# Optimization experiments

Measured on AMD Instinct MI355X. Metric: run time of the kernel, lower is better.

The kernel has to match this reference:

```python
import jax, jax.numpy as jnp
import numpy as np

COMMITMENT_COST = 0.25


def setup_inputs() -> dict:
    key = jax.random.key(0)
    k1, k2 = jax.random.split(key)
    B, L, D, K = 32, 1024, 128, 1024
    z = jax.random.normal(k1, (B, L, D), dtype=jnp.float32)
    # torch init: uniform_(-1/num_embeddings, 1/num_embeddings)
    codebook = jax.random.uniform(k2, (K, D), dtype=jnp.float32,
                                  minval=-1.0 / K, maxval=1.0 / K)
    return {"z": z, "codebook": codebook}


def reference(z, codebook):
    D = codebook.shape[1]
    flat_z = z.reshape(-1, D)                         # [N, D]
    # squared-euclidean distances, expanded form (same math as torch)
    distances = (jnp.sum(flat_z ** 2, axis=1, keepdims=True)
                 + jnp.sum(codebook ** 2, axis=1)
                 - 2.0 * flat_z @ codebook.T)         # [N, K]
    encoding_indices = jnp.argmin(distances, axis=1)  # [N]
    quantized = codebook[encoding_indices].reshape(z.shape)
    # straight-through estimator
    z_q = z + jax.lax.stop_gradient(quantized - z)
    q_loss = jnp.mean((jax.lax.stop_gradient(quantized) - z) ** 2)
    e_loss = jnp.mean((quantized - jax.lax.stop_gradient(z)) ** 2)
    vq_loss = q_loss + COMMITMENT_COST * e_loss
    return z_q, vq_loss, encoding_indices
```

## Files before the change

kernel.cpp:

```cpp
#include <hip/hip_runtime.h>
#include <float.h>

#define NTOK 32768
#define DDIM 128
#define KCODES 1024
#define TT 128
#define KC 64
#define NCHUNK (KCODES / KC)
#define NTHR 512

typedef __attribute__((ext_vector_type(8))) short short8v;
typedef __attribute__((ext_vector_type(4))) float f32x4;

__device__ __forceinline__ float nofuse(float x) { asm volatile("" : "+v"(x)); return x; }

__device__ __forceinline__ unsigned short bf16rne(float x) {
    unsigned int u = __float_as_uint(x);
    unsigned int r = u + 0x7FFFu + ((u >> 16) & 1u);
    return (unsigned short)(r >> 16);
}
__device__ __forceinline__ float bf16tof(unsigned short h) {
    return __uint_as_float(((unsigned int)h) << 16);
}

__device__ __forceinline__ void cvt8(const float* f, uint4& hw, uint4& lw) {
    unsigned int h[8], l[8];
    #pragma unroll
    for (int e = 0; e < 8; ++e) {
        unsigned short hh = bf16rne(f[e]);
        unsigned short ll = bf16rne(f[e] - bf16tof(hh));
        h[e] = hh; l[e] = ll;
    }
    hw = make_uint4(h[0] | (h[1] << 16), h[2] | (h[3] << 16),
                    h[4] | (h[5] << 16), h[6] | (h[7] << 16));
    lw = make_uint4(l[0] | (l[1] << 16), l[2] | (l[3] << 16),
                    l[4] | (l[5] << 16), l[6] | (l[7] << 16));
}

__global__ void rownorm_np(const float* __restrict__ a, float* __restrict__ out, int nrows) {
    int row = blockIdx.x * blockDim.x + threadIdx.x;
    if (row >= nrows) return;
    const float* p = a + (size_t)row * DDIM;
    float r[8];
    #pragma unroll
    for (int j = 0; j < 8; ++j) { float v = p[j]; r[j] = nofuse(v * v); }
    #pragma unroll
    for (int i = 8; i < DDIM; i += 8) {
        #pragma unroll
        for (int j = 0; j < 8; ++j) {
            float v = p[i + j];
            r[j] = nofuse(r[j] + nofuse(v * v));
        }
    }
    float s01 = nofuse(r[0] + r[1]);
    float s23 = nofuse(r[2] + r[3]);
    float s45 = nofuse(r[4] + r[5]);
    float s67 = nofuse(r[6] + r[7]);
    out[row] = nofuse(nofuse(s01 + s23) + nofuse(s45 + s67));
}

__global__ __launch_bounds__(NTHR, 2)
void dist_argmin(const float* __restrict__ z, const float* __restrict__ cb,
                 const float* __restrict__ cnorm,
                 float* __restrict__ zq, float* __restrict__ idxf_out,
                 float* __restrict__ partials) {
    __shared__ __align__(16) char smem[2 * 32768 + 2 * 16384 + 512];
    char* ztH = smem;
    char* ztL = smem + 32768;
    char* ctH = smem + 65536;
    char* ctL = smem + 65536 + 16384;
    float* zn_s = (float*)(smem + 65536 + 32768);
    float* red_v = (float*)ctH;
    int*   red_i = (int*)(ctH + 2048);
    int*   bidx  = (int*)(ctH + 4096);

    const int tid  = threadIdx.x;
    const int lane = tid & 63;
    const int wave = tid >> 6;
    const int wy   = wave & 3;
    const int wx   = wave >> 2;
    const int l15  = lane & 15;
    const int l4   = lane >> 4;
    const int t0   = blockIdx.x * TT;

    float4 pf[4];
    #pragma unroll
    for (int it = 0; it < 2; ++it) {
        int gd = it * NTHR + tid;
        int row = gd >> 4, slot = gd & 15;
        const float* g = cb + (size_t)row * DDIM + slot * 8;
        pf[2 * it]     = *(const float4*)g;
        pf[2 * it + 1] = *(const float4*)(g + 4);
    }

    #pragma unroll
    for (int it = 0; it < 4; ++it) {
        int g = it * NTHR + tid;
        int row = g >> 4, d8 = g & 15;
        const float* p = z + (size_t)(t0 + row) * DDIM + d8 * 8;
        float4 a = *(const float4*)p;
        float4 b = *(const float4*)(p + 4);
        float f[8] = {a.x, a.y, a.z, a.w, b.x, b.y, b.z, b.w};
        uint4 hw, lw;
        cvt8(f, hw, lw);
        int off = row * 256 + ((d8 << 4) ^ ((row & 7) << 4));
        *(uint4*)(ztH + off) = hw;
        *(uint4*)(ztL + off) = lw;
    }

    if (tid < TT) {
        const float* p = z + (size_t)(t0 + tid) * DDIM;
        float r[8];
        {
            float4 a = *(const float4*)p, b = *(const float4*)(p + 4);
            float v[8] = {a.x, a.y, a.z, a.w, b.x, b.y, b.z, b.w};
            #pragma unroll
            for (int j = 0; j < 8; ++j) r[j] = nofuse(v[j] * v[j]);
        }
        #pragma unroll
        for (int i = 8; i < DDIM; i += 8) {
            float4 a = *(const float4*)(p + i), b = *(const float4*)(p + i + 4);
            float v[8] = {a.x, a.y, a.z, a.w, b.x, b.y, b.z, b.w};
            #pragma unroll
            for (int j = 0; j < 8; ++j) r[j] = nofuse(r[j] + nofuse(v[j] * v[j]));
        }
        float s01 = nofuse(r[0] + r[1]), s23 = nofuse(r[2] + r[3]);
        float s45 = nofuse(r[4] + r[5]), s67 = nofuse(r[6] + r[7]);
        zn_s[tid] = nofuse(nofuse(s01 + s23) + nofuse(s45 + s67));
    }
    __syncthreads();

    short8v Ah[2][4], Al[2][4];
    #pragma unroll
    for (int tf = 0; tf < 2; ++tf) {
        int row = wy * 32 + tf * 16 + l15;
        int swz = (row & 7) << 4;
        #pragma unroll
        for (int ks = 0; ks < 4; ++ks) {
            int off = row * 256 + ((ks * 64 + (l4 << 4)) ^ swz);
            Ah[tf][ks] = *(const short8v*)(ztH + off);
            Al[tf][ks] = *(const short8v*)(ztL + off);
        }
    }
    float znr[8];
    #pragma unroll
    for (int tf = 0; tf < 2; ++tf)
        #pragma unroll
        for (int rg = 0; rg < 4; ++rg)
            znr[tf * 4 + rg] = zn_s[wy * 32 + tf * 16 + l4 * 4 + rg];

    float minv[8]; int mini[8];
    #pragma unroll
    for (int i = 0; i < 8; ++i) { minv[i] = FLT_MAX; mini[i] = 0; }

    for (int cc = 0; cc < NCHUNK; ++cc) {
        const int kc = cc * KC;
        __syncthreads();
        #pragma unroll
        for (int it = 0; it < 2; ++it) {
            int gd = it * NTHR + tid;
            int row = gd >> 4, slot = gd & 15;
            float f[8] = {pf[2*it].x, pf[2*it].y, pf[2*it].z, pf[2*it].w,
                          pf[2*it+1].x, pf[2*it+1].y, pf[2*it+1].z, pf[2*it+1].w};
            uint4 hw, lw;
            cvt8(f, hw, lw);
            int off = row * 256 + ((slot << 4) ^ ((row & 7) << 4));
            *(uint4*)(ctH + off) = hw;
            *(uint4*)(ctL + off) = lw;
        }
        __syncthreads();
        if (cc + 1 < NCHUNK) {
            #pragma unroll
            for (int it = 0; it < 2; ++it) {
                int gd = it * NTHR + tid;
                int row = gd >> 4, slot = gd & 15;
                const float* g = cb + (size_t)(kc + KC + row) * DDIM + slot * 8;
                pf[2 * it]     = *(const float4*)g;
                pf[2 * it + 1] = *(const float4*)(g + 4);
            }
        }

        f32x4 acc[2][2];
        #pragma unroll
        for (int tf = 0; tf < 2; ++tf)
            #pragma unroll
            for (int cf = 0; cf < 2; ++cf)
                acc[tf][cf] = (f32x4){0.f, 0.f, 0.f, 0.f};

        #pragma unroll
        for (int ks = 0; ks < 4; ++ks) {
            short8v Bh[2], Bl[2];
            #pragma unroll
            for (int cf = 0; cf < 2; ++cf) {
                int row = wx * 32 + cf * 16 + l15;
                int off = row * 256 + ((ks * 64 + (l4 << 4)) ^ ((row & 7) << 4));
                Bh[cf] = *(const short8v*)(ctH + off);
                Bl[cf] = *(const short8v*)(ctL + off);
            }
            #pragma unroll
            for (int tf = 0; tf < 2; ++tf)
                #pragma unroll
                for (int cf = 0; cf < 2; ++cf) {
                    acc[tf][cf] = __builtin_amdgcn_mfma_f32_16x16x32_bf16(Ah[tf][ks], Bh[cf], acc[tf][cf], 0, 0, 0);
                    acc[tf][cf] = __builtin_amdgcn_mfma_f32_16x16x32_bf16(Ah[tf][ks], Bl[cf], acc[tf][cf], 0, 0, 0);
                    acc[tf][cf] = __builtin_amdgcn_mfma_f32_16x16x32_bf16(Al[tf][ks], Bh[cf], acc[tf][cf], 0, 0, 0);
                }
        }

        #pragma unroll
        for (int cf = 0; cf < 2; ++cf) {
            int kk = kc + wx * 32 + cf * 16 + l15;
            float cn = cnorm[kk];
            #pragma unroll
            for (int tf = 0; tf < 2; ++tf)
                #pragma unroll
                for (int rg = 0; rg < 4; ++rg) {
                    float s = nofuse(znr[tf * 4 + rg] + cn);
                    float dist = fmaf(-2.0f, acc[tf][cf][rg], s);
                    int ii = tf * 4 + rg;
                    if (dist < minv[ii]) { minv[ii] = dist; mini[ii] = kk; }
                }
        }
    }

    __syncthreads();
    #pragma unroll
    for (int i = 0; i < 8; ++i) {
        float bv = minv[i]; int bi = mini[i];
        #pragma unroll
        for (int off = 1; off < 16; off <<= 1) {
            float ov = __shfl_xor(bv, off);
            int   oi = __shfl_xor(bi, off);
            if (ov < bv || (ov == bv && oi < bi)) { bv = ov; bi = oi; }
        }
        if (l15 == 0) {
            int tok = wy * 32 + (i >> 2) * 16 + l4 * 4 + (i & 3);
            red_v[tok * 2 + wx] = bv;
            red_i[tok * 2 + wx] = bi;
        }
    }
    __syncthreads();
    if (tid < TT) {
        float bv = red_v[tid * 2]; int bi = red_i[tid * 2];
        float v1 = red_v[tid * 2 + 1]; int i1 = red_i[tid * 2 + 1];
        if (v1 < bv || (v1 == bv && i1 < bi)) { bv = v1; bi = i1; }
        bidx[tid] = bi;
        idxf_out[t0 + tid] = (float)bi;
    }
    __syncthreads();

    float s = 0.0f;
    #pragma unroll
    for (int ft = 0; ft < 8; ++ft) {
        int g = ft * NTHR + tid;
        int t = g >> 5;
        int d4 = g & 31;
        int k = bidx[t];
        float4 q4 = *(const float4*)(cb + (size_t)k * DDIM + 4 * d4);
        float4 z4 = *(const float4*)(z + (size_t)(t0 + t) * DDIM + 4 * d4);
        *(float4*)(zq + (size_t)(t0 + t) * DDIM + 4 * d4) = q4;
        float dx = q4.x - z4.x, dy = q4.y - z4.y, dz = q4.z - z4.z, dw = q4.w - z4.w;
        s += dx * dx + dy * dy + dz * dz + dw * dw;
    }
    #pragma unroll
    for (int off = 32; off > 0; off >>= 1) s += __shfl_down(s, off);
    __shared__ float sm[8];
    if ((tid & 63) == 0) sm[tid >> 6] = s;
    __syncthreads();
    if (tid == 0) {
        float tot = 0.0f;
        #pragma unroll
        for (int w = 0; w < 8; ++w) tot += sm[w];
        partials[blockIdx.x] = tot;
    }
}

__global__ void loss_final(const float* __restrict__ partials, float* __restrict__ out_loss) {
    double s = 0.0;
    for (int i = threadIdx.x; i < NTOK / TT; i += 256) s += (double)partials[i];
    #pragma unroll
    for (int off = 32; off > 0; off >>= 1) s += __shfl_down(s, off);
    __shared__ double sm[4];
    int lane = threadIdx.x & 63, wv = threadIdx.x >> 6;
    if (lane == 0) sm[wv] = s;
    __syncthreads();
    if (threadIdx.x == 0) {
        double tot = sm[0] + sm[1] + sm[2] + sm[3];
        out_loss[0] = (float)(tot * 1.25 / (double)((size_t)NTOK * DDIM));
    }
}

extern "C" void kernel_launch(void* const* d_in, const int* in_sizes, int n_in,
                              void* d_out, int out_size, void* d_ws, size_t ws_size,
                              hipStream_t stream) {
    const float* z  = (const float*)d_in[0];
    const float* cb = (const float*)d_in[1];
    float* out = (float*)d_out;
    float* zq   = out;
    float* loss = out + (size_t)NTOK * DDIM;
    float* idxf = loss + 1;

    float* cnorm    = (float*)d_ws;
    float* partials = cnorm + KCODES;

    rownorm_np<<<KCODES / 256, 256, 0, stream>>>(cb, cnorm, KCODES);
    dist_argmin<<<NTOK / TT, NTHR, 0, stream>>>(z, cb, cnorm, zq, idxf, partials);
    loss_final<<<1, 256, 0, stream>>>(partials, loss);
}
```

Before: 131.7 us.

## Pre-pack codebook to bf16 hi/lo in global, load MFMA operands directly to registers

Result: slower. 158.1 us (+20.0%).

```diff
diff --git a/kernel.cpp b/kernel.cpp
--- a/kernel.cpp
+++ b/kernel.cpp
@@ -5,8 +5,6 @@
 #define DDIM 128
 #define KCODES 1024
 #define TT 128
-#define KC 64
-#define NCHUNK (KCODES / KC)
 #define NTHR 512
 
 typedef __attribute__((ext_vector_type(8))) short short8v;
@@ -37,42 +35,60 @@
                     l[4] | (l[5] << 16), l[6] | (l[7] << 16));
 }
 
-__global__ void rownorm_np(const float* __restrict__ a, float* __restrict__ out, int nrows) {
-    int row = blockIdx.x * blockDim.x + threadIdx.x;
-    if (row >= nrows) return;
-    const float* p = a + (size_t)row * DDIM;
-    float r[8];
-    #pragma unroll
-    for (int j = 0; j < 8; ++j) { float v = p[j]; r[j] = nofuse(v * v); }
-    #pragma unroll
-    for (int i = 8; i < DDIM; i += 8) {
-        #pragma unroll
-        for (int j = 0; j < 8; ++j) {
-            float v = p[i + j];
-            r[j] = nofuse(r[j] + nofuse(v * v));
-        }
-    }
-    float s01 = nofuse(r[0] + r[1]);
-    float s23 = nofuse(r[2] + r[3]);
-    float s45 = nofuse(r[4] + r[5]);
-    float s67 = nofuse(r[6] + r[7]);
-    out[row] = nofuse(nofuse(s01 + s23) + nofuse(s45 + s67));
+__device__ __forceinline__ short8v as_s8(uint4 v) { return __builtin_bit_cast(short8v, v); }
+
+__global__ __launch_bounds__(256)
+void pack_cb(const float* __restrict__ cb, float* __restrict__ cnorm,
+             ushort* __restrict__ cbh, ushort* __restrict__ cbl) {
+    const int tid = threadIdx.x;
+    const int b = blockIdx.x;
+    {
+        int row = b * 256 + tid;
+        const float* p = cb + (size_t)row * DDIM;
+        float r[8];
+        {
+            float4 a = *(const float4*)p, c = *(const float4*)(p + 4);
+            float v[8] = {a.x, a.y, a.z, a.w, c.x, c.y, c.z, c.w};
+            #pragma unroll
+            for (int j = 0; j < 8; ++j) r[j] = nofuse(v[j] * v[j]);
+        }
+        #pragma unroll
+        for (int i = 8; i < DDIM; i += 8) {
+            float4 a = *(const float4*)(p + i), c = *(const float4*)(p + i + 4);
+            float v[8] = {a.x, a.y, a.z, a.w, c.x, c.y, c.z, c.w};
+            #pragma unroll
+            for (int j = 0; j < 8; ++j) r[j] = nofuse(r[j] + nofuse(v[j] * v[j]));
+        }
+        float s01 = nofuse(r[0] + r[1]), s23 = nofuse(r[2] + r[3]);
+        float s45 = nofuse(r[4] + r[5]), s67 = nofuse(r[6] + r[7]);
+        cnorm[row] = nofuse(nofuse(s01 + s23) + nofuse(s45 + s67));
+    }
+    #pragma unroll
+    for (int it = 0; it < 16; ++it) {
+        int g = it * 256 + tid;
+        int row = b * 256 + (g >> 4);
+        int d8 = g & 15;
+        const float* q = cb + (size_t)row * DDIM + d8 * 8;
+        float4 a = *(const float4*)q, c = *(const float4*)(q + 4);
+        float f[8] = {a.x, a.y, a.z, a.w, c.x, c.y, c.z, c.w};
+        uint4 hw, lw;
+        cvt8(f, hw, lw);
+        *(uint4*)(cbh + (size_t)row * DDIM + d8 * 8) = hw;
+        *(uint4*)(cbl + (size_t)row * DDIM + d8 * 8) = lw;
+    }
 }
 
 __global__ __launch_bounds__(NTHR, 2)
 void dist_argmin(const float* __restrict__ z, const float* __restrict__ cb,
                  const float* __restrict__ cnorm,
+                 const ushort* __restrict__ cbh, const ushort* __restrict__ cbl,
                  float* __restrict__ zq, float* __restrict__ idxf_out,
                  float* __restrict__ partials) {
-    __shared__ __align__(16) char smem[2 * 32768 + 2 * 16384 + 512];
-    char* ztH = smem;
-    char* ztL = smem + 32768;
-    char* ctH = smem + 65536;
-    char* ctL = smem + 65536 + 16384;
-    float* zn_s = (float*)(smem + 65536 + 32768);
-    float* red_v = (float*)ctH;
-    int*   red_i = (int*)(ctH + 2048);
-    int*   bidx  = (int*)(ctH + 4096);
+    __shared__ float zn_s[TT];
+    __shared__ float red_v[TT * 2];
+    __shared__ int   red_i[TT * 2];
+    __shared__ int   bidx[TT];
+    __shared__ float sm[8];
 
     const int tid  = threadIdx.x;
     const int lane = tid & 63;
@@ -83,44 +99,36 @@
     const int l4   = lane >> 4;
     const int t0   = blockIdx.x * TT;
 
-    float4 pf[4];
-    #pragma unroll
-    for (int it = 0; it < 2; ++it) {
-        int gd = it * NTHR + tid;
-        int row = gd >> 4, slot = gd & 15;
-        const float* g = cb + (size_t)row * DDIM + slot * 8;
-        pf[2 * it]     = *(const float4*)g;
-        pf[2 * it + 1] = *(const float4*)(g + 4);
-    }
-
-    #pragma unroll
-    for (int it = 0; it < 4; ++it) {
-        int g = it * NTHR + tid;
-        int row = g >> 4, d8 = g & 15;
-        const float* p = z + (size_t)(t0 + row) * DDIM + d8 * 8;
-        float4 a = *(const float4*)p;
-        float4 b = *(const float4*)(p + 4);
-        float f[8] = {a.x, a.y, a.z, a.w, b.x, b.y, b.z, b.w};
-        uint4 hw, lw;
-        cvt8(f, hw, lw);
-        int off = row * 256 + ((d8 << 4) ^ ((row & 7) << 4));
-        *(uint4*)(ztH + off) = hw;
-        *(uint4*)(ztL + off) = lw;
+    short8v Ah[2][4], Al[2][4];
+    #pragma unroll
+    for (int tf = 0; tf < 2; ++tf) {
+        int row = t0 + wy * 32 + tf * 16 + l15;
+        const float* p = z + (size_t)row * DDIM;
+        #pragma unroll
+        for (int ks = 0; ks < 4; ++ks) {
+            float4 a = *(const float4*)(p + ks * 32 + l4 * 8);
+            float4 c = *(const float4*)(p + ks * 32 + l4 * 8 + 4);
+            float f[8] = {a.x, a.y, a.z, a.w, c.x, c.y, c.z, c.w};
+            uint4 hw, lw;
+            cvt8(f, hw, lw);
+            Ah[tf][ks] = as_s8(hw);
+            Al[tf][ks] = as_s8(lw);
+        }
     }
 
     if (tid < TT) {
         const float* p = z + (size_t)(t0 + tid) * DDIM;
         float r[8];
         {
-            float4 a = *(const float4*)p, b = *(const float4*)(p + 4);
-            float v[8] = {a.x, a.y, a.z, a.w, b.x, b.y, b.z, b.w};
+            float4 a = *(const float4*)p, c = *(const float4*)(p + 4);
+            float v[8] = {a.x, a.y, a.z, a.w, c.x, c.y, c.z, c.w};
             #pragma unroll
             for (int j = 0; j < 8; ++j) r[j] = nofuse(v[j] * v[j]);
         }
         #pragma unroll
         for (int i = 8; i < DDIM; i += 8) {
-            float4 a = *(const float4*)(p + i), b = *(const float4*)(p + i + 4);
-            float v[8] = {a.x, a.y, a.z, a.w, b.x, b.y, b.z, b.w};
+            float4 a = *(const float4*)(p + i), c = *(const float4*)(p + i + 4);
+            float v[8] = {a.x, a.y, a.z, a.w, c.x, c.y, c.z, c.w};
             #pragma unroll
             for (int j = 0; j < 8; ++j) r[j] = nofuse(r[j] + nofuse(v[j] * v[j]));
         }
@@ -130,18 +138,6 @@
     }
     __syncthreads();
 
-    short8v Ah[2][4], Al[2][4];
-    #pragma unroll
-    for (int tf = 0; tf < 2; ++tf) {
-        int row = wy * 32 + tf * 16 + l15;
-        int swz = (row & 7) << 4;
-        #pragma unroll
-        for (int ks = 0; ks < 4; ++ks) {
-            int off = row * 256 + ((ks * 64 + (l4 << 4)) ^ swz);
-            Ah[tf][ks] = *(const short8v*)(ztH + off);
-            Al[tf][ks] = *(const short8v*)(ztL + off);
-        }
-    }
     float znr[8];
     #pragma unroll
     for (int tf = 0; tf < 2; ++tf)
@@ -153,63 +149,42 @@
     #pragma unroll
     for (int i = 0; i < 8; ++i) { minv[i] = FLT_MAX; mini[i] = 0; }
 
-    for (int cc = 0; cc < NCHUNK; ++cc) {
-        const int kc = cc * KC;
-        __syncthreads();
-        #pragma unroll
-        for (int it = 0; it < 2; ++it) {
-            int gd = it * NTHR + tid;
-            int row = gd >> 4, slot = gd & 15;
-            float f[8] = {pf[2*it].x, pf[2*it].y, pf[2*it].z, pf[2*it].w,
-                          pf[2*it+1].x, pf[2*it+1].y, pf[2*it+1].z, pf[2*it+1].w};
-            uint4 hw, lw;
-            cvt8(f, hw, lw);
-            int off = row * 256 + ((slot << 4) ^ ((row & 7) << 4));
-            *(uint4*)(ctH + off) = hw;
-            *(uint4*)(ctL + off) = lw;
-        }
-        __syncthreads();
-        if (cc + 1 < NCHUNK) {
-            #pragma unroll
-            for (int it = 0; it < 2; ++it) {
-                int gd = it * NTHR + tid;
-                int row = gd >> 4, slot = gd & 15;
-                const float* g = cb + (size_t)(kc + KC + row) * DDIM + slot * 8;
-                pf[2 * it]     = *(const float4*)g;
-                pf[2 * it + 1] = *(const float4*)(g + 4);
+    const size_t boff = (size_t)(wx * 32 + l15) * DDIM + l4 * 8;
+
+    short8v B0h[2][4], B0l[2][4], B1h[2][4], B1l[2][4];
+
+    auto loadB = [&](short8v (&Bh)[2][4], short8v (&Bl)[2][4], int it) {
+        const ushort* ph = cbh + (size_t)it * 64 * DDIM + boff;
+        const ushort* pl = cbl + (size_t)it * 64 * DDIM + boff;
+        #pragma unroll
+        for (int cf = 0; cf < 2; ++cf)
+            #pragma unroll
+            for (int ks = 0; ks < 4; ++ks) {
+                Bh[cf][ks] = *(const short8v*)(ph + cf * 16 * DDIM + ks * 32);
+                Bl[cf][ks] = *(const short8v*)(pl + cf * 16 * DDIM + ks * 32);
             }
-        }
-
+    };
+
+    auto compute = [&](short8v (&Bh)[2][4], short8v (&Bl)[2][4], int it) {
         f32x4 acc[2][2];
         #pragma unroll
         for (int tf = 0; tf < 2; ++tf)
             #pragma unroll
             for (int cf = 0; cf < 2; ++cf)
                 acc[tf][cf] = (f32x4){0.f, 0.f, 0.f, 0.f};
-
-        #pragma unroll
-        for (int ks = 0; ks < 4; ++ks) {
-            short8v Bh[2], Bl[2];
-            #pragma unroll
-            for (int cf = 0; cf < 2; ++cf) {
-                int row = wx * 32 + cf * 16 + l15;
-                int off = row * 256 + ((ks * 64 + (l4 << 4)) ^ ((row & 7) << 4));
-                Bh[cf] = *(const short8v*)(ctH + off);
-                Bl[cf] = *(const short8v*)(ctL + off);
-            }
+        #pragma unroll
+        for (int ks = 0; ks < 4; ++ks)
             #pragma unroll
             for (int tf = 0; tf < 2; ++tf)
                 #pragma unroll
                 for (int cf = 0; cf < 2; ++cf) {
-                    acc[tf][cf] = __builtin_amdgcn_mfma_f32_16x16x32_bf16(Ah[tf][ks], Bh[cf], acc[tf][cf], 0, 0, 0);
-                    acc[tf][cf] = __builtin_amdgcn_mfma_f32_16x16x32_bf16(Ah[tf][ks], Bl[cf], acc[tf][cf], 0, 0, 0);
-                    acc[tf][cf] = __builtin_amdgcn_mfma_f32_16x16x32_bf16(Al[tf][ks], Bh[cf], acc[tf][cf], 0, 0, 0);
+                    acc[tf][cf] = __builtin_amdgcn_mfma_f32_16x16x32_bf16(Ah[tf][ks], Bh[cf][ks], acc[tf][cf], 0, 0, 0);
+                    acc[tf][cf] = __builtin_amdgcn_mfma_f32_16x16x32_bf16(Ah[tf][ks], Bl[cf][ks], acc[tf][cf], 0, 0, 0);
+                    acc[tf][cf] = __builtin_amdgcn_mfma_f32_16x16x32_bf16(Al[tf][ks], Bh[cf][ks], acc[tf][cf], 0, 0, 0);
                 }
-        }
-
         #pragma unroll
         for (int cf = 0; cf < 2; ++cf) {
-            int kk = kc + wx * 32 + cf * 16 + l15;
+            int kk = it * 64 + wx * 32 + cf * 16 + l15;
             float cn = cnorm[kk];
             #pragma unroll
             for (int tf = 0; tf < 2; ++tf)
@@ -221,9 +196,17 @@
                     if (dist < minv[ii]) { minv[ii] = dist; mini[ii] = kk; }
                 }
         }
-    }
-
-    __syncthreads();
+    };
+
+    loadB(B0h, B0l, 0);
+    #pragma unroll 1
+    for (int it = 0; it < 16; it += 2) {
+        loadB(B1h, B1l, it + 1);
+        compute(B0h, B0l, it);
+        if (it + 2 < 16) loadB(B0h, B0l, it + 2);
+        compute(B1h, B1l, it + 1);
+    }
+
     #pragma unroll
     for (int i = 0; i < 8; ++i) {
         float bv = minv[i]; int bi = mini[i];
@@ -264,7 +247,6 @@
     }
     #pragma unroll
     for (int off = 32; off > 0; off >>= 1) s += __shfl_down(s, off);
-    __shared__ float sm[8];
     if ((tid & 63) == 0) sm[tid >> 6] = s;
     __syncthreads();
     if (tid == 0) {
@@ -300,10 +282,12 @@
     float* loss = out + (size_t)NTOK * DDIM;
     float* idxf = loss + 1;
 
-    float* cnorm    = (float*)d_ws;
-    float* partials = cnorm + KCODES;
-
-    rownorm_np<<<KCODES / 256, 256, 0, stream>>>(cb, cnorm, KCODES);
-    dist_argmin<<<NTOK / TT, NTHR, 0, stream>>>(z, cb, cnorm, zq, idxf, partials);
+    float*  cnorm    = (float*)d_ws;
+    float*  partials = cnorm + KCODES;
+    ushort* cbh      = (ushort*)(partials + 256);
+    ushort* cbl      = cbh + (size_t)KCODES * DDIM;
+
+    pack_cb<<<KCODES / 256, 256, 0, stream>>>(cb, cnorm, cbh, cbl);
+    dist_argmin<<<NTOK / TT, NTHR, 0, stream>>>(z, cb, cnorm, cbh, cbl, zq, idxf, partials);
     loss_final<<<1, 256, 0, stream>>>(partials, loss);
 }
```
